# Performance work log

Hardware: AMD Instinct MI355X
Metric: run time of the kernel (lower is better)

The kernel has to match this reference:

```python
import jax, jax.numpy as jnp
import numpy as np

BLOCK_SIZE = 2048
HEAD_SIZE = 64
N_EMBD = 768


def setup_inputs() -> dict:
    key = jax.random.key(0)
    k1, k2, k3 = jax.random.split(key, 3)
    x = jax.random.normal(k1, (8, 2048, N_EMBD), dtype=jnp.float32)
    Wq = jax.random.normal(k2, (N_EMBD, HEAD_SIZE), dtype=jnp.float32) * (N_EMBD ** -0.5)
    rel_table = jax.random.normal(k3, (2 * BLOCK_SIZE - 1, 1), dtype=jnp.float32)
    return {"x": x, "Wq": Wq, "rel_table": rel_table}


def reference(x, Wq, rel_table):
    B, T, C = x.shape
    # NOTE: original module uses self.query for q, k AND v (faithful reproduction)
    q = x @ Wq  # [B, T, H]
    k = q
    v = q
    max_rel = BLOCK_SIZE - 1
    pos = jnp.arange(T)
    rel = pos[None, :] - pos[:, None]            # [T, T]
    rel_idx = jnp.clip(rel, -max_rel, max_rel) + max_rel
    bias = rel_table[rel_idx, 0][None, :, :]     # [1, T, T]
    scores = jnp.einsum('bth,bsh->bts', q, k) * (HEAD_SIZE ** -0.5)
    scores = scores + bias
    causal = pos[None, :] <= pos[:, None]        # [T, T] lower-triangular
    scores = jnp.where(causal[None, :, :], scores, -jnp.inf)
    attn = jax.nn.softmax(scores, axis=-1)       # dropout p=0.0 -> identity
    out = jnp.einsum('bts,bsh->bth', attn, v)    # [B, T, H]
    return out
```

## Files before the change

kernel.cpp:

```cpp
#include <hip/hip_runtime.h>
#include <hip/hip_fp16.h>

typedef _Float16 half8 __attribute__((ext_vector_type(8)));
typedef _Float16 half4 __attribute__((ext_vector_type(4)));
typedef float floatx4 __attribute__((ext_vector_type(4)));

#define T_SEQ 2048
#define NB    8

__global__ __launch_bounds__(64) void prep_kernel(
    const float* __restrict__ Wq, _Float16* __restrict__ WqTs)
{
  const int b = blockIdx.x;
  const int cg = b >> 2, t = b & 3;
  const int l = threadIdx.x, n = l & 15, q = l >> 4;
  const int h = 16 * t + n;
  half8 v;
  #pragma unroll
  for (int j = 0; j < 8; ++j)
    v[j] = (_Float16)Wq[(32 * cg + 8 * q + j) * 64 + h];
  *(half8*)(WqTs + (size_t)b * 512 + l * 8) = v;
}

__global__ __launch_bounds__(256, 4) void qproj_kernel(
    const float* __restrict__ x, const _Float16* __restrict__ WqTs,
    const float* __restrict__ rel,
    _Float16* __restrict__ q16, _Float16* __restrict__ q16T,
    float* __restrict__ Ct)
{
  __shared__ __align__(16) char smem[24704];
  _Float16* xs   = (_Float16*)smem;
  float*    cbuf = (float*)smem;
  _Float16* qs   = (_Float16*)(smem + 16640);
  float*    sq   = (float*)(smem + 16640 + 2112);

  const int tid  = threadIdx.x;
  const int w    = tid >> 6, lane = tid & 63;
  const int n    = lane & 15, quad = lane >> 4;
  const int r0   = blockIdx.x * 16;

  #pragma unroll
  for (int i = 0; i < 12; ++i) {
    const int e   = tid + 256 * i;
    const int row = e / 192, c4 = e - row * 192;
    float4 v = *(const float4*)(x + (size_t)(r0 + row) * 768 + 4 * c4);
    half4 hv;
    hv[0] = (_Float16)v.x; hv[1] = (_Float16)v.y;
    hv[2] = (_Float16)v.z; hv[3] = (_Float16)v.w;
    *(half4*)(xs + row * 770 + 4 * c4) = hv;
  }
  __syncthreads();

  floatx4 acc[4];
  #pragma unroll
  for (int s = 0; s < 4; ++s) acc[s] = (floatx4){0.f, 0.f, 0.f, 0.f};

  const int k0 = w * 192;
  #pragma unroll
  for (int c = 0; c < 6; ++c) {
    const int cg = w * 6 + c;
    const _Float16* bp = WqTs + (size_t)cg * 2048 + lane * 8;
    half8 b0 = *(const half8*)(bp);
    half8 b1 = *(const half8*)(bp + 512);
    half8 b2 = *(const half8*)(bp + 1024);
    half8 b3 = *(const half8*)(bp + 1536);
    half8 a  = *(const half8*)(xs + n * 770 + k0 + 32 * c + 8 * quad);
    acc[0] = __builtin_amdgcn_mfma_f32_16x16x32_f16(a, b0, acc[0], 0, 0, 0);
    acc[1] = __builtin_amdgcn_mfma_f32_16x16x32_f16(a, b1, acc[1], 0, 0, 0);
    acc[2] = __builtin_amdgcn_mfma_f32_16x16x32_f16(a, b2, acc[2], 0, 0, 0);
    acc[3] = __builtin_amdgcn_mfma_f32_16x16x32_f16(a, b3, acc[3], 0, 0, 0);
  }
  __syncthreads();

  #pragma unroll
  for (int sub = 0; sub < 4; ++sub)
    #pragma unroll
    for (int r = 0; r < 4; ++r)
      cbuf[w * 1040 + (4 * quad + r) * 65 + sub * 16 + n] = acc[sub][r];
  __syncthreads();

  const float b0v = rel[2047] * 1.44269504f;
  #pragma unroll
  for (int k = 0; k < 4; ++k) {
    const int e = tid + 256 * k;
    const int row = e >> 6, h = e & 63;
    float s = cbuf[row * 65 + h]        + cbuf[1040 + row * 65 + h] +
              cbuf[2080 + row * 65 + h] + cbuf[3120 + row * 65 + h];
    q16[(size_t)(r0 + row) * 64 + h] = (_Float16)s;
    qs[row * 66 + h] = (_Float16)s;
    float ss = s * s;
    #pragma unroll
    for (int off = 1; off < 64; off <<= 1) ss += __shfl_xor(ss, off);
    if (lane == 0) sq[row] = ss;
  }
  __syncthreads();

  if (tid < 16)
    Ct[r0 + tid] = sq[tid] * 0.18033688f + b0v + 8.0f;

  {
    const int h = tid >> 2, rq = (tid & 3) * 4;
    half4 hv;
    hv[0] = qs[(rq + 0) * 66 + h]; hv[1] = qs[(rq + 1) * 66 + h];
    hv[2] = qs[(rq + 2) * 66 + h]; hv[3] = qs[(rq + 3) * 66 + h];
    const int bb = r0 >> 11, tt = r0 & 2047;
    *(half4*)(q16T + (size_t)(bb * 64 + h) * T_SEQ + tt + rq) = hv;
  }
}

__global__ __launch_bounds__(256, 2) void attn_kernel(
    const _Float16* __restrict__ q16, const _Float16* __restrict__ q16T,
    const float* __restrict__ rel, const float* __restrict__ Ct,
    float* __restrict__ out)
{
  __shared__ __align__(16) _Float16 Pbuf[4 * 16 * 72];
  __shared__ float Obuf[4 * 16 * 65];
  __shared__ float Lbuf[4 * 16];
  __shared__ float biasL[2080];

  const int bi = blockIdx.x;
  const int b  = bi & 7;
  const int u  = bi >> 3;
  const int qi = (u < 64) ? u : 191 - u;
  const int t0 = qi * 16;
  const int kfull = t0 >> 6;

  const int tid  = threadIdx.x;
  const int w    = tid >> 6;
  const int lane = tid & 63;
  const int n    = lane & 15, quad = lane >> 4;

  {
    const int lo = 2032 - t0, cnt = t0 + 31;
    for (int i = tid; i < cnt; i += 256) biasL[i] = rel[lo + i] * 1.44269504f;
  }

  half8 aq0, aq1;
  {
    const _Float16* qrow = q16 + (size_t)(b * T_SEQ + t0 + n) * 64 + quad * 8;
    aq0 = *(const half8*)qrow;
    aq1 = *(const half8*)(qrow + 32);
  }
  float ctv[4];
  #pragma unroll
  for (int r = 0; r < 4; ++r)
    ctv[r] = Ct[b * T_SEQ + t0 + 4 * quad + r];

  floatx4 O[4];
  #pragma unroll
  for (int s = 0; s < 4; ++s) O[s] = (floatx4){0.f, 0.f, 0.f, 0.f};
  floatx4 den = (floatx4){0.f, 0.f, 0.f, 0.f};
  const half8 ones = {(_Float16)1, (_Float16)1, (_Float16)1, (_Float16)1,
                      (_Float16)1, (_Float16)1, (_Float16)1, (_Float16)1};

  _Float16* Pw = Pbuf + w * 1152;
  const float ksc = 0.125f * 1.44269504f;
  const _Float16* vbase = q16T + (size_t)(b * 64 + n) * T_SEQ + quad * 8;

  __syncthreads();

  #define LOAD_KV(S0, K, V)                                                   \
    {                                                                         \
      _Pragma("unroll")                                                       \
      for (int sub = 0; sub < 4; ++sub) {                                     \
        const _Float16* kp =                                                  \
            q16 + (size_t)(b * T_SEQ + (S0) + sub * 16 + n) * 64 + quad * 8;  \
        K[2 * sub]     = *(const half8*)kp;                                   \
        K[2 * sub + 1] = *(const half8*)(kp + 32);                            \
      }                                                                       \
      _Pragma("unroll")                                                       \
      for (int sh = 0; sh < 4; ++sh) {                                        \
        V[sh]     = *(const half8*)(vbase + (size_t)(sh * 16) * T_SEQ + (S0));\
        V[4 + sh] = *(const half8*)(vbase + (size_t)(sh * 16) * T_SEQ + (S0) + 32); \
      }                                                                       \
    }

  half8 cK[8], cV[8], nK[8], nV[8];
  int kt = w;
  if (kt <= kfull) LOAD_KV(kt * 64, cK, cV);

  for (; kt <= kfull; kt += 4) {
    const int ktn = kt + 4;
    if (ktn <= kfull) LOAD_KV(ktn * 64, nK, nV);

    const int  s0 = kt * 64;
    const bool dg = (kt == kfull);
    const int  j  = (t0 - s0) >> 4;

    #pragma unroll
    for (int sub = 0; sub < 4; ++sub) {
      if (dg && sub > j) {
        #pragma unroll
        for (int r = 0; r < 4; ++r)
          Pw[(4 * quad + r) * 72 + sub * 16 + n] = (_Float16)0.f;
        continue;
      }
      floatx4 sc = (floatx4){0.f, 0.f, 0.f, 0.f};
      sc = __builtin_amdgcn_mfma_f32_16x16x32_f16(aq0, cK[2 * sub], sc, 0, 0, 0);
      sc = __builtin_amdgcn_mfma_f32_16x16x32_f16(aq1, cK[2 * sub + 1], sc, 0, 0, 0);
      const int smin = s0 + sub * 16;
      #pragma unroll
      for (int r = 0; r < 4; ++r) {
        float bv = biasL[15 + smin + n - 4 * quad - r];
        float pv = exp2f(fmaf(sc[r], ksc, bv) - ctv[r]);
        if (dg && sub == j && n > 4 * quad + r) pv = 0.f;
        Pw[(4 * quad + r) * 72 + sub * 16 + n] = (_Float16)pv;
      }
    }

    #pragma unroll
    for (int ch = 0; ch < 2; ++ch) {
      half8 pf = *(const half8*)(Pw + n * 72 + ch * 32 + quad * 8);
      den = __builtin_amdgcn_mfma_f32_16x16x32_f16(pf, ones, den, 0, 0, 0);
      #pragma unroll
      for (int sh = 0; sh < 4; ++sh)
        O[sh] = __builtin_amdgcn_mfma_f32_16x16x32_f16(pf, cV[ch * 4 + sh],
                                                       O[sh], 0, 0, 0);
    }

    #pragma unroll
    for (int i = 0; i < 8; ++i) { cK[i] = nK[i]; cV[i] = nV[i]; }
  }
  #undef LOAD_KV

  #pragma unroll
  for (int sub = 0; sub < 4; ++sub)
    #pragma unroll
    for (int r = 0; r < 4; ++r)
      Obuf[w * 1040 + (4 * quad + r) * 65 + sub * 16 + n] = O[sub][r];
  if (n == 0) {
    #pragma unroll
    for (int r = 0; r < 4; ++r)
      Lbuf[w * 16 + 4 * quad + r] = den[r];
  }
  __syncthreads();

  #pragma unroll
  for (int k = 0; k < 4; ++k) {
    const int e = tid + k * 256;
    const int row = e >> 6, h = e & 63;
    float num = Obuf[row * 65 + h]        + Obuf[1040 + row * 65 + h] +
                Obuf[2080 + row * 65 + h] + Obuf[3120 + row * 65 + h];
    float d   = Lbuf[row] + Lbuf[16 + row] + Lbuf[32 + row] + Lbuf[48 + row];
    out[(size_t)(b * T_SEQ + t0 + row) * 64 + h] = num / d;
  }
}

extern "C" void kernel_launch(void* const* d_in, const int* in_sizes, int n_in,
                              void* d_out, int out_size, void* d_ws, size_t ws_size,
                              hipStream_t stream) {
  const float* x   = (const float*)d_in[0];
  const float* Wq  = (const float*)d_in[1];
  const float* rel = (const float*)d_in[2];
  float* out = (float*)d_out;

  _Float16* q16   = (_Float16*)d_ws;
  _Float16* q16T  = q16  + (size_t)NB * T_SEQ * 64;
  _Float16* WqTs  = q16T + (size_t)NB * T_SEQ * 64;
  float*    Ct    = (float*)(WqTs + 96 * 512);

  prep_kernel <<<96,    64, 0, stream>>>(Wq, WqTs);
  qproj_kernel<<<1024, 256, 0, stream>>>(x, WqTs, rel, q16, q16T, Ct);
  attn_kernel <<<1024, 256, 0, stream>>>(q16, q16T, rel, Ct, out);
}
```

Baseline: 129.1 us.

## Store Q/K and V in MFMA fragment-ordered layouts for coalesced lane loads

The projection kernel now writes q and its transposed copy directly in the per-lane fragment order consumed by the MFMA operands. Each lane's half8 load in the attention kernel then becomes a contiguous 1KB-per-wavefront access instead of strided row or column gathers. This reduces memory transactions and address arithmetic in the attention inner loop. The cost is a more complex scatter in qproj, including an 8-element column gather from shared memory for the V layout.

```diff
diff --git a/kernel.cpp b/kernel.cpp
--- a/kernel.cpp
+++ b/kernel.cpp
@@ -25,14 +25,14 @@
 __global__ __launch_bounds__(256, 4) void qproj_kernel(
     const float* __restrict__ x, const _Float16* __restrict__ WqTs,
     const float* __restrict__ rel,
-    _Float16* __restrict__ q16, _Float16* __restrict__ q16T,
+    _Float16* __restrict__ q16F, _Float16* __restrict__ v16F,
     float* __restrict__ Ct)
 {
   __shared__ __align__(16) char smem[24704];
   _Float16* xs   = (_Float16*)smem;
   float*    cbuf = (float*)smem;
   _Float16* qs   = (_Float16*)(smem + 16640);
-  float*    sq   = (float*)(smem + 16640 + 2112);
+  float*    sq   = (float*)(smem + 16640 + 2304);
 
   const int tid  = threadIdx.x;
   const int w    = tid >> 6, lane = tid & 63;
@@ -86,8 +86,7 @@
     const int row = e >> 6, h = e & 63;
     float s = cbuf[row * 65 + h]        + cbuf[1040 + row * 65 + h] +
               cbuf[2080 + row * 65 + h] + cbuf[3120 + row * 65 + h];
-    q16[(size_t)(r0 + row) * 64 + h] = (_Float16)s;
-    qs[row * 66 + h] = (_Float16)s;
+    qs[row * 72 + h] = (_Float16)s;
     float ss = s * s;
     #pragma unroll
     for (int off = 1; off < 64; off <<= 1) ss += __shfl_xor(ss, off);
@@ -98,18 +97,28 @@
   if (tid < 16)
     Ct[r0 + tid] = sq[tid] * 0.18033688f + b0v + 8.0f;
 
-  {
-    const int h = tid >> 2, rq = (tid & 3) * 4;
-    half4 hv;
-    hv[0] = qs[(rq + 0) * 66 + h]; hv[1] = qs[(rq + 1) * 66 + h];
-    hv[2] = qs[(rq + 2) * 66 + h]; hv[3] = qs[(rq + 3) * 66 + h];
-    const int bb = r0 >> 11, tt = r0 & 2047;
-    *(half4*)(q16T + (size_t)(bb * 64 + h) * T_SEQ + tt + rq) = hv;
+  if (tid < 128) {
+    const int ch = tid >> 6, l = tid & 63;
+    half8 f = *(const half8*)(qs + (l & 15) * 72 + ch * 32 + (l >> 4) * 8);
+    *(half8*)(q16F + ((size_t)(r0 >> 4) * 2 + ch) * 512 + l * 8) = f;
+  } else {
+    const int u = tid - 128, h = u >> 1, p = u & 1;
+    const int mg = r0 >> 4;
+    const int b  = mg >> 7, ml = mg & 127;
+    const int kt = ml >> 2, chv = (ml >> 1) & 1, q = 2 * (ml & 1) + p;
+    half8 f;
+    #pragma unroll
+    for (int j = 0; j < 8; ++j)
+      f[j] = qs[(8 * p + j) * 72 + h];
+    const size_t off =
+        ((((size_t)(b * 32 + kt) * 2 + chv) * 4 + (h >> 4)) * 64 +
+         ((h & 15) + 16 * q)) * 8;
+    *(half8*)(v16F + off) = f;
   }
 }
 
 __global__ __launch_bounds__(256, 2) void attn_kernel(
-    const _Float16* __restrict__ q16, const _Float16* __restrict__ q16T,
+    const _Float16* __restrict__ q16F, const _Float16* __restrict__ v16F,
     const float* __restrict__ rel, const float* __restrict__ Ct,
     float* __restrict__ out)
 {
@@ -135,11 +144,14 @@
     for (int i = tid; i < cnt; i += 256) biasL[i] = rel[lo + i] * 1.44269504f;
   }
 
+  const _Float16* kfbase = q16F + (size_t)(b * 128) * 1024 + lane * 8;
+  const _Float16* vfbase = v16F + (size_t)(b * 32) * 4096 + lane * 8;
+
   half8 aq0, aq1;
   {
-    const _Float16* qrow = q16 + (size_t)(b * T_SEQ + t0 + n) * 64 + quad * 8;
-    aq0 = *(const half8*)qrow;
-    aq1 = *(const half8*)(qrow + 32);
+    const _Float16* qf = q16F + ((size_t)(b * 128 + (t0 >> 4))) * 1024 + lane * 8;
+    aq0 = *(const half8*)qf;
+    aq1 = *(const half8*)(qf + 512);
   }
   float ctv[4];
   #pragma unroll
@@ -155,33 +167,32 @@
 
   _Float16* Pw = Pbuf + w * 1152;
   const float ksc = 0.125f * 1.44269504f;
-  const _Float16* vbase = q16T + (size_t)(b * 64 + n) * T_SEQ + quad * 8;
-
-  __syncthreads();
-
-  #define LOAD_KV(S0, K, V)                                                   \
+
+  __syncthreads();
+
+  #define LOAD_KV(KT, K, V)                                                   \
     {                                                                         \
+      const _Float16* kp = kfbase + (size_t)(KT) * 4096;                      \
       _Pragma("unroll")                                                       \
       for (int sub = 0; sub < 4; ++sub) {                                     \
-        const _Float16* kp =                                                  \
-            q16 + (size_t)(b * T_SEQ + (S0) + sub * 16 + n) * 64 + quad * 8;  \
-        K[2 * sub]     = *(const half8*)kp;                                   \
-        K[2 * sub + 1] = *(const half8*)(kp + 32);                            \
+        K[2 * sub]     = *(const half8*)(kp + sub * 1024);                    \
+        K[2 * sub + 1] = *(const half8*)(kp + sub * 1024 + 512);              \
       }                                                                       \
+      const _Float16* vp = vfbase + (size_t)(KT) * 4096;                      \
       _Pragma("unroll")                                                       \
       for (int sh = 0; sh < 4; ++sh) {                                        \
-        V[sh]     = *(const half8*)(vbase + (size_t)(sh * 16) * T_SEQ + (S0));\
-        V[4 + sh] = *(const half8*)(vbase + (size_t)(sh * 16) * T_SEQ + (S0) + 32); \
+        V[sh]     = *(const half8*)(vp + sh * 512);                           \
+        V[4 + sh] = *(const half8*)(vp + 2048 + sh * 512);                    \
       }                                                                       \
     }
 
   half8 cK[8], cV[8], nK[8], nV[8];
   int kt = w;
-  if (kt <= kfull) LOAD_KV(kt * 64, cK, cV);
+  if (kt <= kfull) LOAD_KV(kt, cK, cV);
 
   for (; kt <= kfull; kt += 4) {
     const int ktn = kt + 4;
-    if (ktn <= kfull) LOAD_KV(ktn * 64, nK, nV);
+    if (ktn <= kfull) LOAD_KV(ktn, nK, nV);
 
     const int  s0 = kt * 64;
     const bool dg = (kt == kfull);
@@ -254,12 +265,12 @@
   const float* rel = (const float*)d_in[2];
   float* out = (float*)d_out;
 
-  _Float16* q16   = (_Float16*)d_ws;
-  _Float16* q16T  = q16  + (size_t)NB * T_SEQ * 64;
-  _Float16* WqTs  = q16T + (size_t)NB * T_SEQ * 64;
-  float*    Ct    = (float*)(WqTs + 96 * 512);
+  _Float16* q16F = (_Float16*)d_ws;
+  _Float16* v16F = q16F + (size_t)NB * 128 * 1024;
+  _Float16* WqTs = v16F + (size_t)NB * 32 * 4096;
+  float*    Ct   = (float*)(WqTs + 96 * 512);
 
   prep_kernel <<<96,    64, 0, stream>>>(Wq, WqTs);
-  qproj_kernel<<<1024, 256, 0, stream>>>(x, WqTs, rel, q16, q16T, Ct);
-  attn_kernel <<<1024, 256, 0, stream>>>(q16, q16T, rel, Ct, out);
-}
+  qproj_kernel<<<1024, 256, 0, stream>>>(x, WqTs, rel, q16F, v16F, Ct);
+  attn_kernel <<<1024, 256, 0, stream>>>(q16F, v16F, rel, Ct, out);
+}
```

Measured after the change: 111.7 us. 13.4% less time.
